# Performance work log

Measured on AMD Instinct MI355X. Metric: run time of the kernel, lower is better.

Reference implementation:

```python
import jax, jax.numpy as jnp
import numpy as np

N_NODES = 50000


def gcn_conv(x, W, b, src, dst, n_nodes):
    """PyG GCNConv: add self-loops, symmetric norm, linear, scatter-add, bias."""
    h = x @ W  # [N, out]
    # degree with self-loops: deg[i] = 1 + (# edges with dst == i)
    deg = 1.0 + jax.ops.segment_sum(jnp.ones_like(dst, dtype=h.dtype), dst,
                                    num_segments=n_nodes)
    dinv = jax.lax.rsqrt(deg)  # deg^{-1/2}
    # per-edge norm for non-self-loop edges
    norm = dinv[src] * dinv[dst]  # [E]
    agg = jax.ops.segment_sum(h[src] * norm[:, None], dst,
                              num_segments=n_nodes)
    # self-loop contribution: dinv[i]*dinv[i]*h[i] = h[i]/deg[i]
    agg = agg + h * (dinv * dinv)[:, None]
    return agg + b


def setup_inputs() -> dict:
    key = jax.random.key(0)
    ks = jax.random.split(key, 6)
    x = jax.random.normal(ks[0], (N_NODES, 512), dtype=jnp.float32)
    edge_index = jax.random.randint(ks[1], (2, 800000), 0, N_NODES,
                                    dtype=jnp.int64)
    W1 = jax.random.normal(ks[2], (512, 256), dtype=jnp.float32) * (512 ** -0.5)
    b1 = jnp.zeros((256,), dtype=jnp.float32)
    W2 = jax.random.normal(ks[3], (256, 256), dtype=jnp.float32) * (256 ** -0.5)
    b2 = jnp.zeros((256,), dtype=jnp.float32)
    W3 = jax.random.normal(ks[4], (256, 64), dtype=jnp.float32) * (256 ** -0.5)
    b3 = jnp.zeros((64,), dtype=jnp.float32)
    return {"x": x, "edge_index": edge_index, "W1": W1, "b1": b1,
            "W2": W2, "b2": b2, "W3": W3, "b3": b3}


def reference(x, edge_index, W1, b1, W2, b2, W3, b3):
    src, dst = edge_index[0], edge_index[1]
    n = x.shape[0]
    h = gcn_conv(x, W1, b1, src, dst, n)
    h = jax.nn.relu(h)  # dropout is a no-op in eval mode
    h = gcn_conv(h, W2, b2, src, dst, n)
    h = jax.nn.relu(h)
    h = gcn_conv(h, W3, b3, src, dst, n)
    # faithful to the original: softmax then log_softmax
    h = jax.nn.softmax(h, axis=1)
    return jax.nn.log_softmax(h, axis=1)
```

## Files before the change

### kernel.cpp

```cpp
#include <hip/hip_runtime.h>
#include <cstdint>
#include <cstddef>

typedef float  f32x4  __attribute__((ext_vector_type(4)));
typedef float  f32x2  __attribute__((ext_vector_type(2)));

__device__ __forceinline__ unsigned int f2fp8x4(float a, float b, float c, float d) {
  int v = __builtin_amdgcn_cvt_pk_fp8_f32(a, b, 0, false);
  v = __builtin_amdgcn_cvt_pk_fp8_f32(c, d, v, true);
  return (unsigned int)v;
}
__device__ __forceinline__ unsigned char f2fp8(float f) {
  return (unsigned char)(__builtin_amdgcn_cvt_pk_fp8_f32(f, f, 0, false) & 0xff);
}
__device__ __forceinline__ void fp8x8_to_f32(uint2 d, float* f) {
  f32x2 a = __builtin_amdgcn_cvt_pk_f32_fp8((int)d.x, false);
  f32x2 b = __builtin_amdgcn_cvt_pk_f32_fp8((int)d.x, true);
  f32x2 c = __builtin_amdgcn_cvt_pk_f32_fp8((int)d.y, false);
  f32x2 e = __builtin_amdgcn_cvt_pk_f32_fp8((int)d.y, true);
  f[0] = a.x; f[1] = a.y; f[2] = b.x; f[3] = b.y;
  f[4] = c.x; f[5] = c.y; f[6] = e.x; f[7] = e.y;
}
__device__ __forceinline__ void fp8x4_to_f32(unsigned int d, float* f) {
  f32x2 a = __builtin_amdgcn_cvt_pk_f32_fp8((int)d, false);
  f32x2 b = __builtin_amdgcn_cvt_pk_f32_fp8((int)d, true);
  f[0] = a.x; f[1] = a.y; f[2] = b.x; f[3] = b.y;
}
__device__ __forceinline__ void fp8x16_to_f32(uint4 d, float* f) {
  uint2 lo; lo.x = d.x; lo.y = d.y;
  uint2 hi; hi.x = d.z; hi.y = d.w;
  fp8x8_to_f32(lo, f);
  fp8x8_to_f32(hi, f + 8);
}

__device__ __forceinline__ void async_copy16(const void* g, void* l) {
  __builtin_amdgcn_global_load_lds(
      (const __attribute__((address_space(1))) unsigned int*)g,
      (__attribute__((address_space(3))) unsigned int*)l, 16, 0, 0);
}

#define NN 50000
#define MPAD 50048
#define NB 196
#define GS (NB * 256)

#define XB_BLOCKS 6256
#define WB_BLOCKS 52

__global__ __launch_bounds__(256) void gcn_prep_k(
    const float* __restrict__ X, unsigned char* __restrict__ x8,
    const float* __restrict__ W1, const float* __restrict__ W2,
    const float* __restrict__ W3,
    unsigned char* __restrict__ W1T8, unsigned char* __restrict__ W2T8,
    unsigned char* __restrict__ W3T8, int* __restrict__ bar) {
  if (blockIdx.x == 0 && threadIdx.x < 8) bar[threadIdx.x] = 0;
  int b = blockIdx.x;
  if (b < XB_BLOCKS) {
    int idx16 = (b * 256 + threadIdx.x) * 16;
    int row = idx16 >> 9;
    uint4 o;
    if (row < NN) {
      const float* s = &X[idx16];
      float4 v0 = *(const float4*)s;
      float4 v1 = *(const float4*)(s + 4);
      float4 v2 = *(const float4*)(s + 8);
      float4 v3 = *(const float4*)(s + 12);
      o.x = f2fp8x4(v0.x, v0.y, v0.z, v0.w);
      o.y = f2fp8x4(v1.x, v1.y, v1.z, v1.w);
      o.z = f2fp8x4(v2.x, v2.y, v2.z, v2.w);
      o.w = f2fp8x4(v3.x, v3.y, v3.z, v3.w);
    } else {
      o = uint4{0, 0, 0, 0};
    }
    *(uint4*)&x8[idx16] = o;
  } else {
    int wb = b - XB_BLOCKS;
    if (wb < 32) {
      int idx16 = (wb * 256 + threadIdx.x) * 16;
      int n = idx16 >> 9;
      float f[16];
#pragma unroll
      for (int j = 0; j < 16; j++) f[j] = W1[(size_t)((idx16 & 511) + j) * 256 + n];
      uint4 o;
      o.x = f2fp8x4(f[0], f[1], f[2], f[3]);
      o.y = f2fp8x4(f[4], f[5], f[6], f[7]);
      o.z = f2fp8x4(f[8], f[9], f[10], f[11]);
      o.w = f2fp8x4(f[12], f[13], f[14], f[15]);
      *(uint4*)&W1T8[idx16] = o;
    } else if (wb < 48) {
      int idx16 = ((wb - 32) * 256 + threadIdx.x) * 16;
      int n = idx16 >> 8;
      float f[16];
#pragma unroll
      for (int j = 0; j < 16; j++) f[j] = W2[(size_t)((idx16 & 255) + j) * 256 + n];
      uint4 o;
      o.x = f2fp8x4(f[0], f[1], f[2], f[3]);
      o.y = f2fp8x4(f[4], f[5], f[6], f[7]);
      o.z = f2fp8x4(f[8], f[9], f[10], f[11]);
      o.w = f2fp8x4(f[12], f[13], f[14], f[15]);
      *(uint4*)&W2T8[idx16] = o;
    } else {
      int idx16 = ((wb - 48) * 256 + threadIdx.x) * 16;
      int n = idx16 >> 8;
      float f[16];
#pragma unroll
      for (int j = 0; j < 16; j++) f[j] = W3[(size_t)((idx16 & 255) + j) * 64 + n];
      uint4 o;
      o.x = f2fp8x4(f[0], f[1], f[2], f[3]);
      o.y = f2fp8x4(f[4], f[5], f[6], f[7]);
      o.z = f2fp8x4(f[8], f[9], f[10], f[11]);
      o.w = f2fp8x4(f[12], f[13], f[14], f[15]);
      *(uint4*)&W3T8[idx16] = o;
    }
  }
}

__device__ __forceinline__ void gbar(int* bar, int target) {
  __syncthreads();
  if (threadIdx.x == 0) {
    __hip_atomic_fetch_add(bar, 1, __ATOMIC_ACQ_REL, __HIP_MEMORY_SCOPE_AGENT);
    while (__hip_atomic_load(bar, __ATOMIC_ACQUIRE, __HIP_MEMORY_SCOPE_AGENT) < target)
      __builtin_amdgcn_s_sleep(2);
  }
  __syncthreads();
}

__global__ __launch_bounds__(256) void gcn_edges_k(
    const int* __restrict__ src, const int* __restrict__ dst, int E,
    int* __restrict__ cnt, int* __restrict__ rs, int* __restrict__ cur,
    float* __restrict__ dinv, int2* __restrict__ e2,
    int* __restrict__ bsum, int* __restrict__ bar) {
  __shared__ int sb[256];
  __shared__ int sc[256];
  const int t = threadIdx.x, b = blockIdx.x;
  const int i = b * 256 + t;

  if (i < NN) cnt[i] = 0;
  gbar(bar, NB);

  for (int e = i; e < E; e += GS) atomicAdd(&cnt[dst[e]], 1);
  gbar(bar, 2 * NB);

  int v = (i < NN) ? cnt[i] : 0;
  sb[t] = v;
  __syncthreads();
  for (int off = 1; off < 256; off <<= 1) {
    int x = (t >= off) ? sb[t - off] : 0;
    __syncthreads();
    sb[t] += x;
    __syncthreads();
  }
  if (t == 255) bsum[b] = sb[255];
  gbar(bar, 3 * NB);

  if (b == 0) {
    int w = (t < NB) ? bsum[t] : 0;
    sc[t] = w;
    __syncthreads();
    for (int off = 1; off < 256; off <<= 1) {
      int x = (t >= off) ? sc[t - off] : 0;
      __syncthreads();
      sc[t] += x;
      __syncthreads();
    }
    if (t < NB) bsum[t] = sc[t] - w;
  }
  gbar(bar, 4 * NB);

  if (i < NN) {
    int off = bsum[b] + sb[t] - v;
    rs[i] = off; cur[i] = off;
    dinv[i] = rsqrtf(1.0f + (float)v);
  }
  if (i == 0) rs[NN] = E;
  gbar(bar, 5 * NB);

  for (int e = i; e < E; e += 4 * GS) {
    int d_[4], s_[4]; bool v_[4];
#pragma unroll
    for (int u = 0; u < 4; u++) {
      int ee = e + u * GS;
      v_[u] = ee < E;
      d_[u] = v_[u] ? dst[ee] : 0;
      s_[u] = v_[u] ? src[ee] : 0;
    }
#pragma unroll
    for (int u = 0; u < 4; u++) {
      if (v_[u]) {
        int p = atomicAdd(&cur[d_[u]], 1);
        int2 w; w.x = s_[u]; w.y = __float_as_int(dinv[s_[u]] * dinv[d_[u]]);
        e2[p] = w;
      }
    }
  }
}

template<int BN, int WTN>
__global__ __launch_bounds__(256) void gcn_gemm_f8_db_k(
    const unsigned char* __restrict__ A8,
    const unsigned char* __restrict__ Bt8,
    unsigned char* __restrict__ C8,
    int K, int N) {
  static_assert(BN == 128, "db kernel assumes uniform 2 global_load_lds per thread");
  __shared__ __align__(16) unsigned char lds_a[2][128 * 32];
  __shared__ __align__(16) unsigned char lds_b[2][BN * 32];
  const int t = threadIdx.x;
  const int wave = t >> 6, lane = t & 63;
  const int wr = wave >> 1, wc = wave & 1;
  const int quad = lane >> 4, lrow = lane & 15;
  const int m0 = blockIdx.x * 128;
  const int n0 = blockIdx.y * BN;

  f32x4 acc[4][WTN] = {};

  auto stage = [&](int buf, int k0) {
    int r = t >> 1, c = (t & 1) * 16;
    async_copy16(&A8[(size_t)(m0 + r) * K + k0 + c], &lds_a[buf][t * 16]);
    int rr = t >> 1, cc = (t & 1) * 16;
    async_copy16(&Bt8[(size_t)(n0 + rr) * K + k0 + cc], &lds_b[buf][t * 16]);
  };
  auto compute = [&](int buf) {
    long af[4], bfr[WTN];
#pragma unroll
    for (int mt = 0; mt < 4; mt++)
      af[mt] = *(const long*)&lds_a[buf][(wr * 64 + mt * 16 + lrow) * 32 + quad * 8];
#pragma unroll
    for (int nt = 0; nt < WTN; nt++)
      bfr[nt] = *(const long*)&lds_b[buf][(wc * (BN / 2) + nt * 16 + lrow) * 32 + quad * 8];
#pragma unroll
    for (int mt = 0; mt < 4; mt++)
#pragma unroll
      for (int nt = 0; nt < WTN; nt++)
        acc[mt][nt] = __builtin_amdgcn_mfma_f32_16x16x32_fp8_fp8(af[mt], bfr[nt], acc[mt][nt], 0, 0, 0);
  };

  stage(0, 0);
  int curb = 0;
  int k0 = 0;
  for (; k0 + 32 < K; k0 += 32) {
    stage(curb ^ 1, k0 + 32);
    asm volatile("s_waitcnt vmcnt(2)" ::: "memory");
    __builtin_amdgcn_s_barrier();
    asm volatile("" ::: "memory");
    compute(curb);
    asm volatile("" ::: "memory");
    __builtin_amdgcn_s_barrier();
    curb ^= 1;
  }
  asm volatile("s_waitcnt vmcnt(0)" ::: "memory");
  __builtin_amdgcn_s_barrier();
  asm volatile("" ::: "memory");
  compute(curb);

#pragma unroll
  for (int mt = 0; mt < 4; mt++)
#pragma unroll
    for (int nt = 0; nt < WTN; nt++)
#pragma unroll
      for (int r = 0; r < 4; r++) {
        int row = m0 + wr * 64 + mt * 16 + quad * 4 + r;
        int col = n0 + wc * (BN / 2) + nt * 16 + lrow;
        C8[(size_t)row * N + col] = f2fp8(acc[mt][nt][r]);
      }
}

template<int BN, int WTN>
__global__ __launch_bounds__(256) void gcn_gemm_f8_s_k(
    const unsigned char* __restrict__ A8, const unsigned char* __restrict__ Bt8,
    unsigned char* __restrict__ C8, int K, int N) {
  __shared__ __align__(16) unsigned char lds_a[128 * 32];
  __shared__ __align__(16) unsigned char lds_b[BN * 32];
  const int t = threadIdx.x;
  const int wave = t >> 6, lane = t & 63;
  const int wr = wave >> 1, wc = wave & 1;
  const int quad = lane >> 4, lrow = lane & 15;
  const int m0 = blockIdx.x * 128;
  const int n0 = blockIdx.y * BN;

  f32x4 acc[4][WTN] = {};

  for (int k0 = 0; k0 < K; k0 += 32) {
    __syncthreads();
    {
      int r = t >> 1, c = (t & 1) * 16;
      async_copy16(&A8[(size_t)(m0 + r) * K + k0 + c], &lds_a[t * 16]);
    }
    for (int q = t; q < BN * 2; q += 256) {
      int r = q >> 1, c = (q & 1) * 16;
      async_copy16(&Bt8[(size_t)(n0 + r) * K + k0 + c], &lds_b[q * 16]);
    }
    __syncthreads();
    long af[4], bfr[WTN];
#pragma unroll
    for (int mt = 0; mt < 4; mt++)
      af[mt] = *(const long*)&lds_a[(wr * 64 + mt * 16 + lrow) * 32 + quad * 8];
#pragma unroll
    for (int nt = 0; nt < WTN; nt++)
      bfr[nt] = *(const long*)&lds_b[(wc * (BN / 2) + nt * 16 + lrow) * 32 + quad * 8];
#pragma unroll
    for (int mt = 0; mt < 4; mt++)
#pragma unroll
      for (int nt = 0; nt < WTN; nt++)
        acc[mt][nt] = __builtin_amdgcn_mfma_f32_16x16x32_fp8_fp8(af[mt], bfr[nt], acc[mt][nt], 0, 0, 0);
  }

#pragma unroll
  for (int mt = 0; mt < 4; mt++)
#pragma unroll
    for (int nt = 0; nt < WTN; nt++)
#pragma unroll
      for (int r = 0; r < 4; r++) {
        int row = m0 + wr * 64 + mt * 16 + quad * 4 + r;
        int col = n0 + wc * (BN / 2) + nt * 16 + lrow;
        C8[(size_t)row * N + col] = f2fp8(acc[mt][nt][r]);
      }
}

template<int D>
__global__ __launch_bounds__(256) void gcn_agg_relu_k(
    const unsigned char* __restrict__ h8, const int* __restrict__ rs,
    const int2* __restrict__ e2, const float* __restrict__ dinv,
    const float* __restrict__ bias, unsigned char* __restrict__ out8, int nNodes) {
  int wave = threadIdx.x >> 6, lane = threadIdx.x & 63;
  int i = blockIdx.x * 4 + wave;
  if (i >= nNodes) return;
  int q = lane >> 4, sub = lane & 15;
  int f0 = sub * 16;
  float di = dinv[i];
  uint4 dself = *(const uint4*)&h8[(size_t)i * D + f0];
  float sv[16];
  fp8x16_to_f32(dself, sv);
  float wself = (q == 0) ? di * di : 0.0f;
  float acc[16];
#pragma unroll
  for (int j = 0; j < 16; j++) acc[j] = sv[j] * wself;

  int e0 = rs[i], e1 = rs[i + 1];
  int nIter = (e1 - e0 + 15) >> 4;
  int e = e0 + q;
  for (int k = 0; k < nIter; k++) {
    int idx[4]; float w[4];
#pragma unroll
    for (int u = 0; u < 4; u++) {
      int ee = e + 4 * u;
      bool v = ee < e1;
      int2 pr = e2[v ? ee : e0];
      idx[u] = v ? pr.x : i;
      w[u] = v ? __int_as_float(pr.y) : 0.0f;
    }
    uint4 d0 = *(const uint4*)&h8[(size_t)idx[0] * D + f0];
    uint4 d1 = *(const uint4*)&h8[(size_t)idx[1] * D + f0];
    uint4 d2 = *(const uint4*)&h8[(size_t)idx[2] * D + f0];
    uint4 d3 = *(const uint4*)&h8[(size_t)idx[3] * D + f0];
    float r[16];
    fp8x16_to_f32(d0, r);
#pragma unroll
    for (int j = 0; j < 16; j++) acc[j] += r[j] * w[0];
    fp8x16_to_f32(d1, r);
#pragma unroll
    for (int j = 0; j < 16; j++) acc[j] += r[j] * w[1];
    fp8x16_to_f32(d2, r);
#pragma unroll
    for (int j = 0; j < 16; j++) acc[j] += r[j] * w[2];
    fp8x16_to_f32(d3, r);
#pragma unroll
    for (int j = 0; j < 16; j++) acc[j] += r[j] * w[3];
    e += 16;
  }
#pragma unroll
  for (int j = 0; j < 16; j++) {
    acc[j] += __shfl_xor(acc[j], 16);
    acc[j] += __shfl_xor(acc[j], 32);
  }
  if (q == 0) {
    float4 bb0 = *(const float4*)&bias[f0];
    float4 bb1 = *(const float4*)&bias[f0 + 4];
    float4 bb2 = *(const float4*)&bias[f0 + 8];
    float4 bb3 = *(const float4*)&bias[f0 + 12];
    float bv[16] = {bb0.x, bb0.y, bb0.z, bb0.w, bb1.x, bb1.y, bb1.z, bb1.w,
                    bb2.x, bb2.y, bb2.z, bb2.w, bb3.x, bb3.y, bb3.z, bb3.w};
    float r[16];
#pragma unroll
    for (int j = 0; j < 16; j++) {
      float z = acc[j] + bv[j];
      r[j] = z > 0.0f ? z : 0.0f;
    }
    uint4 o;
    o.x = f2fp8x4(r[0], r[1], r[2], r[3]);
    o.y = f2fp8x4(r[4], r[5], r[6], r[7]);
    o.z = f2fp8x4(r[8], r[9], r[10], r[11]);
    o.w = f2fp8x4(r[12], r[13], r[14], r[15]);
    *(uint4*)&out8[(size_t)i * D + f0] = o;
  }
}

__global__ __launch_bounds__(256) void gcn_agg_final_k(
    const unsigned char* __restrict__ h8, const int* __restrict__ rs,
    const int2* __restrict__ e2, const float* __restrict__ dinv,
    const float* __restrict__ bias, float* __restrict__ out, int nNodes) {
  int wave = threadIdx.x >> 6, lane = threadIdx.x & 63;
  int i = blockIdx.x * 4 + wave;
  if (i >= nNodes) return;
  int qtr = lane >> 4, sub = lane & 15;
  int f0 = sub * 4;
  float di = dinv[i];
  unsigned int dself = *(const unsigned int*)&h8[(size_t)i * 64 + f0];
  float sv[4];
  fp8x4_to_f32(dself, sv);
  float wself = (qtr == 0) ? di * di : 0.0f;
  float acc[4];
#pragma unroll
  for (int j = 0; j < 4; j++) acc[j] = sv[j] * wself;

  int e0 = rs[i], e1 = rs[i + 1];
  int nIter = (e1 - e0 + 7) >> 3;
  int e = e0 + qtr;
  for (int k = 0; k < nIter; k++) {
    int idx[2]; float w[2];
#pragma unroll
    for (int u = 0; u < 2; u++) {
      int ee = e + 4 * u;
      bool v = ee < e1;
      int2 pr = e2[v ? ee : e0];
      idx[u] = v ? pr.x : i;
      w[u] = v ? __int_as_float(pr.y) : 0.0f;
    }
    unsigned int d0 = *(const unsigned int*)&h8[(size_t)idx[0] * 64 + f0];
    unsigned int d1 = *(const unsigned int*)&h8[(size_t)idx[1] * 64 + f0];
    float r0[4], r1[4];
    fp8x4_to_f32(d0, r0); fp8x4_to_f32(d1, r1);
#pragma unroll
    for (int j = 0; j < 4; j++)
      acc[j] += r0[j] * w[0] + r1[j] * w[1];
    e += 8;
  }
#pragma unroll
  for (int j = 0; j < 4; j++) {
    acc[j] += __shfl_xor(acc[j], 16);
    acc[j] += __shfl_xor(acc[j], 32);
    acc[j] += bias[f0 + j];
  }
  float m = fmaxf(fmaxf(acc[0], acc[1]), fmaxf(acc[2], acc[3]));
#pragma unroll
  for (int off = 8; off > 0; off >>= 1) m = fmaxf(m, __shfl_xor(m, off));
  float ex[4], s = 0.0f;
#pragma unroll
  for (int j = 0; j < 4; j++) { ex[j] = __expf(acc[j] - m); s += ex[j]; }
#pragma unroll
  for (int off = 8; off > 0; off >>= 1) s += __shfl_xor(s, off);
  float rcs = 1.0f / s;
  float p[4], s2 = 0.0f;
#pragma unroll
  for (int j = 0; j < 4; j++) { p[j] = ex[j] * rcs; s2 += __expf(p[j]); }
#pragma unroll
  for (int off = 8; off > 0; off >>= 1) s2 += __shfl_xor(s2, off);
  float ls = __logf(s2);
  if (qtr == 0) {
    float4 o; o.x = p[0] - ls; o.y = p[1] - ls; o.z = p[2] - ls; o.w = p[3] - ls;
    *(float4*)&out[(size_t)i * 64 + f0] = o;
  }
}

extern "C" void kernel_launch(void* const* d_in, const int* in_sizes, int n_in,
                              void* d_out, int out_size, void* d_ws, size_t ws_size,
                              hipStream_t stream) {
  const float* x    = (const float*)d_in[0];
  const int*   eidx = (const int*)d_in[1];
  const float* W1   = (const float*)d_in[2];
  const float* b1   = (const float*)d_in[3];
  const float* W2   = (const float*)d_in[4];
  const float* b2   = (const float*)d_in[5];
  const float* W3   = (const float*)d_in[6];
  const float* b3   = (const float*)d_in[7];
  float* out = (float*)d_out;

  const int E = in_sizes[1] / 2;
  const int* src = eidx;
  const int* dst = eidx + E;

  char* p = (char*)d_ws;
  auto alloc = [&](size_t bytes) -> void* {
    void* r = (void*)p;
    p += (bytes + 255) & ~(size_t)255;
    return r;
  };
  unsigned char*  x8   = (unsigned char*)alloc((size_t)MPAD * 512);
  unsigned char*  g8   = (unsigned char*)alloc((size_t)MPAD * 256);
  unsigned char*  a8   = (unsigned char*)alloc((size_t)MPAD * 256);
  unsigned char*  g83  = (unsigned char*)alloc((size_t)MPAD * 64);
  unsigned char*  W1T8 = (unsigned char*)alloc((size_t)256 * 512);
  unsigned char*  W2T8 = (unsigned char*)alloc((size_t)256 * 256);
  unsigned char*  W3T8 = (unsigned char*)alloc((size_t)64 * 256);
  int*   cnt  = (int*)alloc((size_t)NN * 4);
  int*   rs   = (int*)alloc((size_t)(NN + 1) * 4);
  int*   cur  = (int*)alloc((size_t)NN * 4);
  float* dinv = (float*)alloc((size_t)NN * 4);
  int2*  e2   = (int2*)alloc((size_t)E * 8);
  int*   bsum = (int*)alloc((size_t)NB * 4);
  int*   bar  = (int*)alloc((size_t)8 * 4);

  gcn_prep_k<<<XB_BLOCKS + WB_BLOCKS, 256, 0, stream>>>(
      x, x8, W1, W2, W3, W1T8, W2T8, W3T8, bar);
  gcn_edges_k<<<NB, 256, 0, stream>>>(src, dst, E, cnt, rs, cur, dinv, e2, bsum, bar);

  const int MB = MPAD / 128;
  gcn_gemm_f8_db_k<128, 4><<<dim3(MB, 2), 256, 0, stream>>>(x8, W1T8, g8, 512, 256);
  gcn_agg_relu_k<256><<<(NN + 3) / 4, 256, 0, stream>>>(g8, rs, e2, dinv, b1, a8, NN);
  gcn_gemm_f8_db_k<128, 4><<<dim3(MB, 2), 256, 0, stream>>>(a8, W2T8, g8, 256, 256);
  gcn_agg_relu_k<256><<<(NN + 3) / 4, 256, 0, stream>>>(g8, rs, e2, dinv, b2, a8, NN);
  gcn_gemm_f8_s_k<64, 2><<<dim3(MB, 1), 256, 0, stream>>>(a8, W3T8, g83, 256, 64);
  gcn_agg_final_k<<<(NN + 3) / 4, 256, 0, stream>>>(g83, rs, e2, dinv, b3, out, NN);

  (void)n_in; (void)out_size; (void)ws_size;
}
```

Baseline: 459.3 us.

## Split persistent edge kernel with grid barriers into separate CSR-build kernels

Replaces the single 196-block persistent edge-processing kernel, which used software grid barriers, with five separate launches: count, block-sum, top-level scan, final scan, and scatter. The count zeroing moves into the prep kernel. The count and scatter phases now run with one thread per edge across many blocks instead of 196 blocks striding, which should raise parallelism for the atomics and remove spin-wait barrier overhead. The cost is extra kernel launches and the loss of the unrolled multi-edge loop in the scatter step.

```diff
diff --git a/kernel.cpp b/kernel.cpp
--- a/kernel.cpp
+++ b/kernel.cpp
@@ -41,8 +41,7 @@
 
 #define NN 50000
 #define MPAD 50048
-#define NB 196
-#define GS (NB * 256)
+#define SCAN_BLOCKS 196
 
 #define XB_BLOCKS 6256
 #define WB_BLOCKS 52
@@ -52,9 +51,12 @@
     const float* __restrict__ W1, const float* __restrict__ W2,
     const float* __restrict__ W3,
     unsigned char* __restrict__ W1T8, unsigned char* __restrict__ W2T8,
-    unsigned char* __restrict__ W3T8, int* __restrict__ bar) {
-  if (blockIdx.x == 0 && threadIdx.x < 8) bar[threadIdx.x] = 0;
+    unsigned char* __restrict__ W3T8, int* __restrict__ cnt) {
   int b = blockIdx.x;
+  if (b < SCAN_BLOCKS) {
+    int ii = b * 256 + threadIdx.x;
+    if (ii < NN) cnt[ii] = 0;
+  }
   if (b < XB_BLOCKS) {
     int idx16 = (b * 256 + threadIdx.x) * 16;
     int row = idx16 >> 9;
@@ -115,33 +117,28 @@
   }
 }
 
-__device__ __forceinline__ void gbar(int* bar, int target) {
+__global__ void gcn_count_k(const int* __restrict__ dst, int* __restrict__ cnt, int E) {
+  int e = blockIdx.x * 256 + threadIdx.x;
+  if (e < E) atomicAdd(&cnt[dst[e]], 1);
+}
+
+__global__ __launch_bounds__(256) void gcn_scan_blocks_k(
+    const int* __restrict__ cnt, int* __restrict__ blockSum, int nNodes) {
+  __shared__ int sw[4];
+  int t = threadIdx.x;
+  int i = blockIdx.x * 256 + t;
+  int v = (i < nNodes) ? cnt[i] : 0;
+  for (int off = 32; off > 0; off >>= 1) v += __shfl_down(v, off);
+  if ((t & 63) == 0) sw[t >> 6] = v;
   __syncthreads();
-  if (threadIdx.x == 0) {
-    __hip_atomic_fetch_add(bar, 1, __ATOMIC_ACQ_REL, __HIP_MEMORY_SCOPE_AGENT);
-    while (__hip_atomic_load(bar, __ATOMIC_ACQUIRE, __HIP_MEMORY_SCOPE_AGENT) < target)
-      __builtin_amdgcn_s_sleep(2);
-  }
-  __syncthreads();
-}
-
-__global__ __launch_bounds__(256) void gcn_edges_k(
-    const int* __restrict__ src, const int* __restrict__ dst, int E,
-    int* __restrict__ cnt, int* __restrict__ rs, int* __restrict__ cur,
-    float* __restrict__ dinv, int2* __restrict__ e2,
-    int* __restrict__ bsum, int* __restrict__ bar) {
+  if (t == 0) blockSum[blockIdx.x] = sw[0] + sw[1] + sw[2] + sw[3];
+}
+
+__global__ __launch_bounds__(256) void gcn_scan_tops_k(
+    int* __restrict__ blockSum, int nBlocks) {
   __shared__ int sb[256];
-  __shared__ int sc[256];
-  const int t = threadIdx.x, b = blockIdx.x;
-  const int i = b * 256 + t;
-
-  if (i < NN) cnt[i] = 0;
-  gbar(bar, NB);
-
-  for (int e = i; e < E; e += GS) atomicAdd(&cnt[dst[e]], 1);
-  gbar(bar, 2 * NB);
-
-  int v = (i < NN) ? cnt[i] : 0;
+  int t = threadIdx.x;
+  int v = (t < nBlocks) ? blockSum[t] : 0;
   sb[t] = v;
   __syncthreads();
   for (int off = 1; off < 256; off <<= 1) {
@@ -150,48 +147,43 @@
     sb[t] += x;
     __syncthreads();
   }
-  if (t == 255) bsum[b] = sb[255];
-  gbar(bar, 3 * NB);
-
-  if (b == 0) {
-    int w = (t < NB) ? bsum[t] : 0;
-    sc[t] = w;
+  if (t < nBlocks) blockSum[t] = sb[t] - v;
+}
+
+__global__ __launch_bounds__(256) void gcn_scan_final_k(
+    const int* __restrict__ cnt, const int* __restrict__ blockSum,
+    int* __restrict__ rs, int* __restrict__ cur, float* __restrict__ dinv,
+    int nNodes, int E) {
+  __shared__ int sb[256];
+  int t = threadIdx.x;
+  int i = blockIdx.x * 256 + t;
+  int v = (i < nNodes) ? cnt[i] : 0;
+  sb[t] = v;
+  __syncthreads();
+  for (int off = 1; off < 256; off <<= 1) {
+    int x = (t >= off) ? sb[t - off] : 0;
     __syncthreads();
-    for (int off = 1; off < 256; off <<= 1) {
-      int x = (t >= off) ? sc[t - off] : 0;
-      __syncthreads();
-      sc[t] += x;
-      __syncthreads();
-    }
-    if (t < NB) bsum[t] = sc[t] - w;
-  }
-  gbar(bar, 4 * NB);
-
-  if (i < NN) {
-    int off = bsum[b] + sb[t] - v;
+    sb[t] += x;
+    __syncthreads();
+  }
+  if (i < nNodes) {
+    int off = blockSum[blockIdx.x] + sb[t] - v;
     rs[i] = off; cur[i] = off;
     dinv[i] = rsqrtf(1.0f + (float)v);
   }
-  if (i == 0) rs[NN] = E;
-  gbar(bar, 5 * NB);
-
-  for (int e = i; e < E; e += 4 * GS) {
-    int d_[4], s_[4]; bool v_[4];
-#pragma unroll
-    for (int u = 0; u < 4; u++) {
-      int ee = e + u * GS;
-      v_[u] = ee < E;
-      d_[u] = v_[u] ? dst[ee] : 0;
-      s_[u] = v_[u] ? src[ee] : 0;
-    }
-#pragma unroll
-    for (int u = 0; u < 4; u++) {
-      if (v_[u]) {
-        int p = atomicAdd(&cur[d_[u]], 1);
-        int2 w; w.x = s_[u]; w.y = __float_as_int(dinv[s_[u]] * dinv[d_[u]]);
-        e2[p] = w;
-      }
-    }
+  if (i == 0) rs[nNodes] = E;
+}
+
+__global__ void gcn_scatter_k(const int* __restrict__ src, const int* __restrict__ dst,
+                              int* __restrict__ cur, const float* __restrict__ dinv,
+                              int2* __restrict__ e2, int E) {
+  int e = blockIdx.x * 256 + threadIdx.x;
+  if (e < E) {
+    int d = dst[e];
+    int s = src[e];
+    int p = atomicAdd(&cur[d], 1);
+    int2 v; v.x = s; v.y = __float_as_int(dinv[s] * dinv[d]);
+    e2[p] = v;
   }
 }
 
@@ -216,8 +208,7 @@
   auto stage = [&](int buf, int k0) {
     int r = t >> 1, c = (t & 1) * 16;
     async_copy16(&A8[(size_t)(m0 + r) * K + k0 + c], &lds_a[buf][t * 16]);
-    int rr = t >> 1, cc = (t & 1) * 16;
-    async_copy16(&Bt8[(size_t)(n0 + rr) * K + k0 + cc], &lds_b[buf][t * 16]);
+    async_copy16(&Bt8[(size_t)(n0 + r) * K + k0 + c], &lds_b[buf][t * 16]);
   };
   auto compute = [&](int buf) {
     long af[4], bfr[WTN];
@@ -496,12 +487,16 @@
   int*   cur  = (int*)alloc((size_t)NN * 4);
   float* dinv = (float*)alloc((size_t)NN * 4);
   int2*  e2   = (int2*)alloc((size_t)E * 8);
-  int*   bsum = (int*)alloc((size_t)NB * 4);
-  int*   bar  = (int*)alloc((size_t)8 * 4);
-
+  int*   bsum = (int*)alloc((size_t)SCAN_BLOCKS * 4);
+
+  const int EB = (E + 255) / 256;
   gcn_prep_k<<<XB_BLOCKS + WB_BLOCKS, 256, 0, stream>>>(
-      x, x8, W1, W2, W3, W1T8, W2T8, W3T8, bar);
-  gcn_edges_k<<<NB, 256, 0, stream>>>(src, dst, E, cnt, rs, cur, dinv, e2, bsum, bar);
+      x, x8, W1, W2, W3, W1T8, W2T8, W3T8, cnt);
+  gcn_count_k<<<EB, 256, 0, stream>>>(dst, cnt, E);
+  gcn_scan_blocks_k<<<SCAN_BLOCKS, 256, 0, stream>>>(cnt, bsum, NN);
+  gcn_scan_tops_k<<<1, 256, 0, stream>>>(bsum, SCAN_BLOCKS);
+  gcn_scan_final_k<<<SCAN_BLOCKS, 256, 0, stream>>>(cnt, bsum, rs, cur, dinv, NN, E);
+  gcn_scatter_k<<<EB, 256, 0, stream>>>(src, dst, cur, dinv, e2, E);
 
   const int MB = MPAD / 128;
   gcn_gemm_f8_db_k<128, 4><<<dim3(MB, 2), 256, 0, stream>>>(x8, W1T8, g8, 512, 256);
```

New measurement: 412.8 us. 1.11x faster.
